# Kernel optimization log

Measured on AMD Instinct MI355X. Metric: run time of the kernel, lower is better.

Reference implementation:

```python
import jax, jax.numpy as jnp
import numpy as np

D_MODEL = 1024
NUM_HEADS = 16
D_HEAD = D_MODEL // NUM_HEADS
MAX_DISTANCE = 128
SEQ_LEN = 2048


def setup_inputs() -> dict:
    key = jax.random.key(0)
    k_x, k_qkv, k_out, k_bias = jax.random.split(key, 4)
    scale = 1.0 / np.sqrt(D_MODEL)
    return {
        "x": jax.random.normal(k_x, (SEQ_LEN, D_MODEL), dtype=jnp.float32),
        "w_qkv": jax.random.normal(k_qkv, (D_MODEL, 3 * D_MODEL), dtype=jnp.float32) * scale,
        "w_out": jax.random.normal(k_out, (D_MODEL, D_MODEL), dtype=jnp.float32) * scale,
        "rel_bias": jax.random.normal(k_bias, (MAX_DISTANCE, NUM_HEADS), dtype=jnp.float32) * 0.02,
    }


def _position_bias(rel_bias, seq_len):
    # relative_position[q, k] = k - q; bucket = clip(|rel|, 0, max_distance-1)
    ctx = jnp.arange(seq_len)[:, None]
    mem = jnp.arange(seq_len)[None, :]
    bucket = jnp.clip(jnp.abs(mem - ctx), 0, MAX_DISTANCE - 1)  # [q, k]
    return rel_bias[bucket]  # [q, k, h]


def reference(x, w_qkv, w_out, rel_bias):
    seq_len = x.shape[0]
    qkv = x @ w_qkv  # [s, 3*d_model]
    q, k, v = jnp.split(qkv, 3, axis=-1)
    q = q.reshape(seq_len, NUM_HEADS, D_HEAD)
    k = k.reshape(seq_len, NUM_HEADS, D_HEAD)
    v = v.reshape(seq_len, NUM_HEADS, D_HEAD)
    bias = _position_bias(rel_bias, seq_len)  # [q, k, h]
    # flax dot_product_attention semantics: scale q by 1/sqrt(d_head), add bias, softmax over kv
    scores = jnp.einsum("qhd,khd->hqk", q, k) / jnp.sqrt(jnp.asarray(D_HEAD, q.dtype))
    scores = scores + jnp.transpose(bias, (2, 0, 1))  # [h, q, k]
    weights = jax.nn.softmax(scores, axis=-1)
    attn = jnp.einsum("hqk,khd->qhd", weights, v)  # [s, h, d_head]
    attn = attn.reshape(1, seq_len, D_MODEL)
    return attn @ w_out  # [1, s, d_model]
```

## Files before the change

### kernel.cpp

```cpp
#include <hip/hip_runtime.h>
#include <hip/hip_bf16.h>

#define SEQ   2048
#define DM    1024
#define NH    16
#define DH    64
#define MAXD  128

#define LOG2E 1.44269504f

typedef __attribute__((ext_vector_type(8))) short  short8;
typedef __attribute__((ext_vector_type(4))) float  float4v;

__device__ __forceinline__ short8 ld8(const void* p) {
    short8 v; __builtin_memcpy(&v, p, 16); return v;
}
__device__ __forceinline__ void st8(void* p, short8 v) {
    __builtin_memcpy(p, &v, 16);
}
__device__ __forceinline__ short bf16bits(float f) {
    __hip_bfloat16 b = __float2bfloat16(f);
    short s; __builtin_memcpy(&s, &b, 2); return s;
}
__device__ __forceinline__ short bf16fast(float f) {
    unsigned u = __builtin_bit_cast(unsigned, f);
    return (short)((u + 0x8000u) >> 16);
}
__device__ __forceinline__ float bits2f(short s) {
    unsigned u = (unsigned)(unsigned short)s << 16;
    return __builtin_bit_cast(float, u);
}
__device__ __forceinline__ short fp16bits(float f) {
    _Float16 h = (_Float16)f; short s; __builtin_memcpy(&s, &h, 2); return s;
}
__device__ __forceinline__ float f16tof(short s) {
    _Float16 h; __builtin_memcpy(&h, &s, 2); return (float)h;
}
__device__ __forceinline__ float fexp2(float x) {
    float r; asm("v_exp_f32 %0, %1" : "=v"(r) : "v"(x)); return r;
}

__device__ __forceinline__ void async16(void* lds, const void* g) {
    __builtin_amdgcn_global_load_lds(
        (const __attribute__((address_space(1))) unsigned int*)g,
        (__attribute__((address_space(3))) unsigned int*)lds, 16, 0, 0);
}

template <int CTRL>
__device__ __forceinline__ float dppmov(float x) {
    return __builtin_bit_cast(float,
        __builtin_amdgcn_update_dpp(0, __builtin_bit_cast(int, x), CTRL, 0xf, 0xf, true));
}
__device__ __forceinline__ float red16max(float x) {
    x = fmaxf(x, dppmov<0xB1>(x));
    x = fmaxf(x, dppmov<0x4E>(x));
    x = fmaxf(x, dppmov<0x141>(x));
    x = fmaxf(x, dppmov<0x140>(x));
    return x;
}
__device__ __forceinline__ float red16sum(float x) {
    x += dppmov<0xB1>(x);
    x += dppmov<0x4E>(x);
    x += dppmov<0x141>(x);
    x += dppmov<0x140>(x);
    return x;
}

__global__ __launch_bounds__(256) void prep_kernel(
    const float* __restrict__ wq, const float* __restrict__ wo,
    const float* __restrict__ x,
    __hip_bfloat16* __restrict__ wqT, __hip_bfloat16* __restrict__ woT,
    __hip_bfloat16* __restrict__ xb) {
    const int t = threadIdx.x;
    const int bx = blockIdx.x;
    if (bx >= 128) {
        const size_t id = (size_t)(bx - 128) * 32 + blockIdx.y;
        const size_t i  = id * 2048 + t * 8;
        float f[8]; __builtin_memcpy(f, x + i, 32);
        short8 v;
#pragma unroll
        for (int j = 0; j < 8; ++j) v[j] = bf16bits(f[j]);
        st8(xb + i, v);
        return;
    }
    __shared__ __hip_bfloat16 tile[32][33];
    const int tx = t % 32, ty = t / 32;
    const int r0 = blockIdx.y * 32;
    const float* src; __hip_bfloat16* dst; int ss, ds, c0;
    if (bx < 96) { src = wq; dst = wqT; ss = 3 * DM; ds = DM; c0 = bx * 32; }
    else         { src = wo; dst = woT; ss = DM;     ds = DM; c0 = (bx - 96) * 32; }
#pragma unroll
    for (int i = 0; i < 4; ++i)
        tile[ty + i * 8][tx] = __float2bfloat16(src[(size_t)(r0 + ty + i * 8) * ss + c0 + tx]);
    __syncthreads();
#pragma unroll
    for (int i = 0; i < 4; ++i)
        dst[(size_t)(c0 + ty + i * 8) * ds + r0 + tx] = tile[tx][ty + i * 8];
}

__global__ __launch_bounds__(256) void gemm_qkv(
    const __hip_bfloat16* __restrict__ A,
    const __hip_bfloat16* __restrict__ BT,
    __hip_bfloat16* __restrict__ C,
    __hip_bfloat16* __restrict__ vTg,
    int M, int N, int K) {
    __shared__ short As[2 * 128 * 32];
    __shared__ short Bs[2 * 64 * 32];
    __shared__ short Tv[64 * 132];

    const int t = threadIdx.x;
    const int w = t >> 6, lane = t & 63;
    const int l15 = lane & 15, quad = lane >> 4;
    const int row0 = blockIdx.y * 128;
    const int col0 = blockIdx.x * 64;
    const int wm = w >> 1, wn = w & 1;

    float4v acc[4][2];
#pragma unroll
    for (int i = 0; i < 4; ++i)
#pragma unroll
        for (int j = 0; j < 2; ++j) acc[i][j] = (float4v){0.f, 0.f, 0.f, 0.f};

    const int mloc0 = lane >> 2;
    const int u     = lane & 3;

    for (int k0 = 0; k0 < K; k0 += 64) {
#pragma unroll
        for (int kc = 0; kc < 2; ++kc) {
#pragma unroll
            for (int i = 0; i < 2; ++i) {
                const int c = 2 * w + i;
                async16(&As[kc * 4096 + c * 512],
                        A + (size_t)(row0 + c * 16 + mloc0) * K + k0 + kc * 32 + u * 8);
            }
            async16(&Bs[kc * 2048 + w * 512],
                    BT + (size_t)(col0 + w * 16 + mloc0) * K + k0 + kc * 32 + u * 8);
        }
        __syncthreads();

#pragma unroll
        for (int kc = 0; kc < 2; ++kc) {
            short8 af[4], bf[2];
#pragma unroll
            for (int mt = 0; mt < 4; ++mt)
                af[mt] = ld8(&As[kc * 4096 + (wm * 64 + mt * 16 + l15) * 32 + quad * 8]);
#pragma unroll
            for (int nt = 0; nt < 2; ++nt)
                bf[nt] = ld8(&Bs[kc * 2048 + (wn * 32 + nt * 16 + l15) * 32 + quad * 8]);
#pragma unroll
            for (int mt = 0; mt < 4; ++mt)
#pragma unroll
                for (int nt = 0; nt < 2; ++nt)
                    acc[mt][nt] = __builtin_amdgcn_mfma_f32_16x16x32_bf16(
                        af[mt], bf[nt], acc[mt][nt], 0, 0, 0);
        }
        __syncthreads();
    }

    if (col0 < 2 * DM) {
#pragma unroll
        for (int mt = 0; mt < 4; ++mt)
#pragma unroll
            for (int nt = 0; nt < 2; ++nt)
#pragma unroll
                for (int r = 0; r < 4; ++r) {
                    const int row = row0 + wm * 64 + mt * 16 + quad * 4 + r;
                    const int col = col0 + wn * 32 + nt * 16 + l15;
                    C[(size_t)row * N + col] = __float2bfloat16(acc[mt][nt][r]);
                }
    } else {
#pragma unroll
        for (int mt = 0; mt < 4; ++mt)
#pragma unroll
            for (int nt = 0; nt < 2; ++nt)
#pragma unroll
                for (int r = 0; r < 4; ++r)
                    Tv[(wn * 32 + nt * 16 + l15) * 132 + wm * 64 + mt * 16 + quad * 4 + r] =
                        bf16bits(acc[mt][nt][r]);
        __syncthreads();
#pragma unroll
        for (int p = 0; p < 4; ++p) {
            const int idx = p * 256 + t;
            const int dl = idx >> 4, uu = idx & 15;
            st8(&vTg[((size_t)(col0 - 2 * DM) + dl) * SEQ + row0 + uu * 8],
                ld8(&Tv[dl * 132 + uu * 8]));
        }
    }
}

__global__ __launch_bounds__(256) void gemm_out(
    const __hip_bfloat16* __restrict__ A,
    const __hip_bfloat16* __restrict__ BT,
    float* __restrict__ C,
    int M, int N, int K) {
    __shared__ short As[2 * 64 * 32];
    __shared__ short Bs[2 * 64 * 32];

    const int t = threadIdx.x;
    const int w = t >> 6, lane = t & 63;
    const int l15 = lane & 15, quad = lane >> 4;
    const int row0 = blockIdx.y * 64;
    const int col0 = blockIdx.x * 64;
    const int wm = w >> 1, wn = w & 1;

    float4v acc[2][2];
#pragma unroll
    for (int i = 0; i < 2; ++i)
#pragma unroll
        for (int j = 0; j < 2; ++j) acc[i][j] = (float4v){0.f, 0.f, 0.f, 0.f};

    const int mloc0 = lane >> 2;
    const int u     = lane & 3;

    for (int k0 = 0; k0 < K; k0 += 64) {
#pragma unroll
        for (int kc = 0; kc < 2; ++kc) {
            async16(&As[kc * 2048 + w * 512],
                    A + (size_t)(row0 + w * 16 + mloc0) * K + k0 + kc * 32 + u * 8);
            async16(&Bs[kc * 2048 + w * 512],
                    BT + (size_t)(col0 + w * 16 + mloc0) * K + k0 + kc * 32 + u * 8);
        }
        __syncthreads();

#pragma unroll
        for (int kc = 0; kc < 2; ++kc) {
            short8 af[2], bf[2];
#pragma unroll
            for (int mt = 0; mt < 2; ++mt)
                af[mt] = ld8(&As[kc * 2048 + (wm * 32 + mt * 16 + l15) * 32 + quad * 8]);
#pragma unroll
            for (int nt = 0; nt < 2; ++nt)
                bf[nt] = ld8(&Bs[kc * 2048 + (wn * 32 + nt * 16 + l15) * 32 + quad * 8]);
#pragma unroll
            for (int mt = 0; mt < 2; ++mt)
#pragma unroll
                for (int nt = 0; nt < 2; ++nt)
                    acc[mt][nt] = __builtin_amdgcn_mfma_f32_16x16x32_bf16(
                        af[mt], bf[nt], acc[mt][nt], 0, 0, 0);
        }
        __syncthreads();
    }

#pragma unroll
    for (int mt = 0; mt < 2; ++mt)
#pragma unroll
        for (int nt = 0; nt < 2; ++nt)
#pragma unroll
            for (int r = 0; r < 4; ++r) {
                const int row = row0 + wm * 32 + mt * 16 + quad * 4 + r;
                const int col = col0 + wn * 32 + nt * 16 + l15;
                C[(size_t)row * N + col] = acc[mt][nt][r];
            }
}

#define TK    128
#define NTILE (SEQ / 2 / TK)
#define KS    68
#define VS    132

__global__ __launch_bounds__(256) void attn_part(
    const __hip_bfloat16* __restrict__ qkv,
    const __hip_bfloat16* __restrict__ vT,
    const float* __restrict__ rel_bias,
    short* __restrict__ opart,
    float* __restrict__ ml) {
    __shared__ short KtPl[TK * KS];
    __shared__ short Vt[DH * VS];
    __shared__ float biasL[MAXD];

    const int t = threadIdx.x;
    const int w = t >> 6, lane = t & 63;
    const int l15 = lane & 15, quad = lane >> 4;

    const int id = blockIdx.x;
    const int qb = (id >> 3) & 31;
    const int c  = (id & 7) + 8 * (id >> 8);
    const int h  = c & 15;
    const int half = c >> 4;
    const int kbase = half * (SEQ / 2);
    const int q0 = qb * 64;
    const int qw = q0 + w * 16;

    if (t < MAXD) biasL[t] = rel_bias[t * NH + h] * LOG2E;

    short8 qf[2];
#pragma unroll
    for (int cc = 0; cc < 2; ++cc) {
        short8 raw = ld8(qkv + (size_t)(qw + l15) * (3 * DM) + h * DH + cc * 32 + quad * 8);
#pragma unroll
        for (int j = 0; j < 8; ++j) qf[cc][j] = bf16bits(bits2f(raw[j]) * (0.125f * LOG2E));
    }

    float4v o_acc[4];
#pragma unroll
    for (int nt = 0; nt < 4; ++nt) o_acc[nt] = (float4v){0.f, 0.f, 0.f, 0.f};
    float m_i[4], l_i[4];
#pragma unroll
    for (int r = 0; r < 4; ++r) { m_i[r] = -1e30f; l_i[r] = 0.f; }

    for (int kb = 0; kb < NTILE; ++kb) {
        const int k0 = kbase + kb * TK;
#pragma unroll
        for (int p = 0; p < 4; ++p) {
            const int idx = p * 256 + t;
            const int row = idx >> 3, u = idx & 7;
            st8(&KtPl[row * KS + u * 8],
                ld8(qkv + (size_t)(k0 + row) * (3 * DM) + DM + h * DH + u * 8));
        }
#pragma unroll
        for (int p = 0; p < 4; ++p) {
            const int idx = p * 256 + t;
            const int row = idx >> 4, u = idx & 15;
            st8(&Vt[row * VS + u * 8],
                ld8(vT + (size_t)(h * DH + row) * SEQ + k0 + u * 8));
        }
        __syncthreads();

        float4v s_acc[8];
#pragma unroll
        for (int kt = 0; kt < 8; ++kt) s_acc[kt] = (float4v){0.f, 0.f, 0.f, 0.f};
#pragma unroll
        for (int cc = 0; cc < 2; ++cc)
#pragma unroll
            for (int kt = 0; kt < 8; ++kt) {
                short8 kf = ld8(&KtPl[(kt * 16 + l15) * KS + (cc * 4 + quad) * 8]);
                s_acc[kt] = __builtin_amdgcn_mfma_f32_16x16x32_bf16(qf[cc], kf, s_acc[kt], 0, 0, 0);
            }

        float sv[8][4];
        const int dlo = k0 - (qw + 15);
        const int dhi = qw - (k0 + TK - 1);
        if (dlo >= MAXD - 1 || dhi >= MAXD - 1) {
            const float bu = biasL[MAXD - 1];
#pragma unroll
            for (int kt = 0; kt < 8; ++kt)
#pragma unroll
                for (int r = 0; r < 4; ++r) sv[kt][r] = s_acc[kt][r] + bu;
        } else {
#pragma unroll
            for (int kt = 0; kt < 8; ++kt)
#pragma unroll
                for (int r = 0; r < 4; ++r) {
                    const int kg = k0 + kt * 16 + l15;
                    const int qg = qw + quad * 4 + r;
                    int rel = kg - qg; if (rel < 0) rel = -rel;
                    if (rel > MAXD - 1) rel = MAXD - 1;
                    sv[kt][r] = s_acc[kt][r] + biasL[rel];
                }
        }

        float rowm[4];
#pragma unroll
        for (int r = 0; r < 4; ++r) {
            float m = sv[0][r];
#pragma unroll
            for (int kt = 1; kt < 8; ++kt) m = fmaxf(m, sv[kt][r]);
            rowm[r] = red16max(m);
        }

        float al[4], rs[4];
#pragma unroll
        for (int r = 0; r < 4; ++r) {
            const float mn = fmaxf(m_i[r], rowm[r]);
            al[r] = fexp2(m_i[r] - mn);
            m_i[r] = mn;
            rs[r] = 0.f;
        }
#pragma unroll
        for (int kt = 0; kt < 8; ++kt)
#pragma unroll
            for (int r = 0; r < 4; ++r) {
                const float p = fexp2(sv[kt][r] - m_i[r]);
                sv[kt][r] = p;
                rs[r] += p;
            }
#pragma unroll
        for (int r = 0; r < 4; ++r) {
            rs[r] = red16sum(rs[r]);
            l_i[r] = l_i[r] * al[r] + rs[r];
        }
#pragma unroll
        for (int nt = 0; nt < 4; ++nt)
#pragma unroll
            for (int r = 0; r < 4; ++r) o_acc[nt][r] *= al[r];

        __syncthreads();

#pragma unroll
        for (int kt = 0; kt < 8; ++kt)
#pragma unroll
            for (int r = 0; r < 4; ++r)
                KtPl[w * 16 * VS + (quad * 4 + r) * VS + kt * 16 + l15] = bf16fast(sv[kt][r]);

#pragma unroll
        for (int kc = 0; kc < 4; ++kc) {
            short8 pf = ld8(&KtPl[w * 16 * VS + l15 * VS + kc * 32 + quad * 8]);
#pragma unroll
            for (int nt = 0; nt < 4; ++nt) {
                short8 vf = ld8(&Vt[(nt * 16 + l15) * VS + kc * 32 + quad * 8]);
                o_acc[nt] = __builtin_amdgcn_mfma_f32_16x16x32_bf16(pf, vf, o_acc[nt], 0, 0, 0);
            }
        }
        __syncthreads();
    }

#pragma unroll
    for (int nt = 0; nt < 4; ++nt)
#pragma unroll
        for (int r = 0; r < 4; ++r) {
            const int row = qw + quad * 4 + r;
            const int col = h * DH + nt * 16 + l15;
            opart[((size_t)half * SEQ + row) * DM + col] = fp16bits(o_acc[nt][r] / l_i[r]);
        }
    if (l15 == 0) {
#pragma unroll
        for (int r = 0; r < 4; ++r) {
            const int row = qw + quad * 4 + r;
            float* mp = ml + (((size_t)half * SEQ + row) * NH + h) * 2;
            mp[0] = m_i[r];
            mp[1] = l_i[r];
        }
    }
}

__global__ __launch_bounds__(256) void combine_kernel(
    const short* __restrict__ opart,
    const float* __restrict__ ml,
    __hip_bfloat16* __restrict__ attnb) {
    const size_t e = ((size_t)blockIdx.x * 256 + threadIdx.x) * 8;
    const int row = (int)(e >> 10);
    const int c0  = (int)(e & 1023);
    const int h   = c0 >> 6;

    const float* mp1 = ml + ((size_t)row * NH + h) * 2;
    const float* mp2 = mp1 + (size_t)SEQ * NH * 2;
    const float m1 = mp1[0], l1 = mp1[1];
    const float m2 = mp2[0], l2 = mp2[1];
    const float mx = fmaxf(m1, m2);
    const float e1 = fexp2(m1 - mx) * l1;
    const float e2 = fexp2(m2 - mx) * l2;
    const float inv = 1.f / (e1 + e2);
    const float w1 = e1 * inv, w2 = e2 * inv;

    short8 a = ld8(opart + (size_t)row * DM + c0);
    short8 b = ld8(opart + (size_t)SEQ * DM + (size_t)row * DM + c0);
    short8 o;
#pragma unroll
    for (int j = 0; j < 8; ++j)
        o[j] = bf16bits(w1 * f16tof(a[j]) + w2 * f16tof(b[j]));
    st8(attnb + (size_t)row * DM + c0, o);
}

extern "C" void kernel_launch(void* const* d_in, const int* in_sizes, int n_in,
                              void* d_out, int out_size, void* d_ws, size_t ws_size,
                              hipStream_t stream) {
    const float* x        = (const float*)d_in[0];
    const float* w_qkv    = (const float*)d_in[1];
    const float* w_out    = (const float*)d_in[2];
    const float* rel_bias = (const float*)d_in[3];
    float* out = (float*)d_out;

    char* p = (char*)d_ws;
    __hip_bfloat16* xb    = (__hip_bfloat16*)p;  p += (size_t)SEQ * DM * 2;
    __hip_bfloat16* wqT   = (__hip_bfloat16*)p;  p += (size_t)3 * DM * DM * 2;
    __hip_bfloat16* woT   = (__hip_bfloat16*)p;  p += (size_t)DM * DM * 2;
    __hip_bfloat16* qkvb  = (__hip_bfloat16*)p;  p += (size_t)SEQ * 3 * DM * 2;
    __hip_bfloat16* vT    = (__hip_bfloat16*)p;  p += (size_t)DM * SEQ * 2;
    __hip_bfloat16* attnb = (__hip_bfloat16*)p;

    short* opart = (short*)d_ws;
    float* ml    = (float*)((char*)d_ws + (size_t)2 * SEQ * DM * 2);

    prep_kernel<<<dim3(160, 32), 256, 0, stream>>>(w_qkv, w_out, x, wqT, woT, xb);

    gemm_qkv<<<dim3(3 * DM / 64, SEQ / 128), 256, 0, stream>>>(
        xb, wqT, qkvb, vT, SEQ, 3 * DM, DM);

    attn_part<<<1024, 256, 0, stream>>>(qkvb, vT, rel_bias, opart, ml);
    combine_kernel<<<1024, 256, 0, stream>>>(opart, ml, attnb);

    gemm_out<<<dim3(DM / 64, SEQ / 64), 256, 0, stream>>>(
        attnb, woT, out, SEQ, DM, DM);
}
```

Baseline: 167.6 us.

## Process 32 query rows per wave with transposed MFMA in split-KV attention

```diff
diff --git a/kernel.cpp b/kernel.cpp
--- a/kernel.cpp
+++ b/kernel.cpp
@@ -22,16 +22,20 @@
     __hip_bfloat16 b = __float2bfloat16(f);
     short s; __builtin_memcpy(&s, &b, 2); return s;
 }
-__device__ __forceinline__ short bf16fast(float f) {
-    unsigned u = __builtin_bit_cast(unsigned, f);
-    return (short)((u + 0x8000u) >> 16);
-}
 __device__ __forceinline__ float bits2f(short s) {
     unsigned u = (unsigned)(unsigned short)s << 16;
     return __builtin_bit_cast(float, u);
 }
-__device__ __forceinline__ short fp16bits(float f) {
-    _Float16 h = (_Float16)f; short s; __builtin_memcpy(&s, &h, 2); return s;
+__device__ __forceinline__ unsigned packbf2(float a, float b) {
+    unsigned ua = (__builtin_bit_cast(unsigned, a) + 0x8000u) >> 16;
+    unsigned ub = (__builtin_bit_cast(unsigned, b) + 0x8000u) & 0xffff0000u;
+    return ua | ub;
+}
+__device__ __forceinline__ unsigned packh2(float a, float b) {
+    _Float16 ha = (_Float16)a, hb = (_Float16)b;
+    unsigned short ua, ub;
+    __builtin_memcpy(&ua, &ha, 2); __builtin_memcpy(&ub, &hb, 2);
+    return (unsigned)ua | ((unsigned)ub << 16);
 }
 __device__ __forceinline__ float f16tof(short s) {
     _Float16 h; __builtin_memcpy(&h, &s, 2); return (float)h;
@@ -44,26 +48,6 @@
     __builtin_amdgcn_global_load_lds(
         (const __attribute__((address_space(1))) unsigned int*)g,
         (__attribute__((address_space(3))) unsigned int*)lds, 16, 0, 0);
-}
-
-template <int CTRL>
-__device__ __forceinline__ float dppmov(float x) {
-    return __builtin_bit_cast(float,
-        __builtin_amdgcn_update_dpp(0, __builtin_bit_cast(int, x), CTRL, 0xf, 0xf, true));
-}
-__device__ __forceinline__ float red16max(float x) {
-    x = fmaxf(x, dppmov<0xB1>(x));
-    x = fmaxf(x, dppmov<0x4E>(x));
-    x = fmaxf(x, dppmov<0x141>(x));
-    x = fmaxf(x, dppmov<0x140>(x));
-    return x;
-}
-__device__ __forceinline__ float red16sum(float x) {
-    x += dppmov<0xB1>(x);
-    x += dppmov<0x4E>(x);
-    x += dppmov<0x141>(x);
-    x += dppmov<0x140>(x);
-    return x;
 }
 
 __global__ __launch_bounds__(256) void prep_kernel(
@@ -257,14 +241,15 @@
 #define NTILE (SEQ / 2 / TK)
 #define KS    68
 #define VS    132
-
-__global__ __launch_bounds__(256) void attn_part(
+#define PS    140
+
+__global__ __launch_bounds__(256, 2) void attn_part(
     const __hip_bfloat16* __restrict__ qkv,
     const __hip_bfloat16* __restrict__ vT,
     const float* __restrict__ rel_bias,
     short* __restrict__ opart,
     float* __restrict__ ml) {
-    __shared__ short KtPl[TK * KS];
+    __shared__ short KtP[4 * 32 * PS];
     __shared__ short Vt[DH * VS];
     __shared__ float biasL[MAXD];
 
@@ -273,30 +258,33 @@
     const int l15 = lane & 15, quad = lane >> 4;
 
     const int id = blockIdx.x;
-    const int qb = (id >> 3) & 31;
-    const int c  = (id & 7) + 8 * (id >> 8);
+    const int qb = (id >> 3) & 15;
+    const int c  = (id & 7) + 8 * (id >> 7);
     const int h  = c & 15;
     const int half = c >> 4;
     const int kbase = half * (SEQ / 2);
-    const int q0 = qb * 64;
-    const int qw = q0 + w * 16;
+    const int qw = qb * 128 + w * 32;
 
     if (t < MAXD) biasL[t] = rel_bias[t * NH + h] * LOG2E;
 
-    short8 qf[2];
-#pragma unroll
-    for (int cc = 0; cc < 2; ++cc) {
-        short8 raw = ld8(qkv + (size_t)(qw + l15) * (3 * DM) + h * DH + cc * 32 + quad * 8);
-#pragma unroll
-        for (int j = 0; j < 8; ++j) qf[cc][j] = bf16bits(bits2f(raw[j]) * (0.125f * LOG2E));
-    }
-
-    float4v o_acc[4];
-#pragma unroll
-    for (int nt = 0; nt < 4; ++nt) o_acc[nt] = (float4v){0.f, 0.f, 0.f, 0.f};
-    float m_i[4], l_i[4];
-#pragma unroll
-    for (int r = 0; r < 4; ++r) { m_i[r] = -1e30f; l_i[r] = 0.f; }
+    short8 qf[2][2];
+#pragma unroll
+    for (int qg = 0; qg < 2; ++qg)
+#pragma unroll
+        for (int cc = 0; cc < 2; ++cc) {
+            short8 raw = ld8(qkv + (size_t)(qw + qg * 16 + l15) * (3 * DM) + h * DH + cc * 32 + quad * 8);
+#pragma unroll
+            for (int j = 0; j < 8; ++j) qf[qg][cc][j] = bf16bits(bits2f(raw[j]) * (0.125f * LOG2E));
+        }
+
+    float4v o_acc[4][2];
+#pragma unroll
+    for (int nt = 0; nt < 4; ++nt)
+#pragma unroll
+        for (int qg = 0; qg < 2; ++qg) o_acc[nt][qg] = (float4v){0.f, 0.f, 0.f, 0.f};
+    float m_i[2] = {-1e30f, -1e30f}, l_i[2] = {0.f, 0.f};
+
+    short* Pw = &KtP[w * 32 * PS];
 
     for (int kb = 0; kb < NTILE; ++kb) {
         const int k0 = kbase + kb * TK;
@@ -304,7 +292,7 @@
         for (int p = 0; p < 4; ++p) {
             const int idx = p * 256 + t;
             const int row = idx >> 3, u = idx & 7;
-            st8(&KtPl[row * KS + u * 8],
+            st8(&KtP[row * KS + u * 8],
                 ld8(qkv + (size_t)(k0 + row) * (3 * DM) + DM + h * DH + u * 8));
         }
 #pragma unroll
@@ -316,109 +304,130 @@
         }
         __syncthreads();
 
-        float4v s_acc[8];
-#pragma unroll
-        for (int kt = 0; kt < 8; ++kt) s_acc[kt] = (float4v){0.f, 0.f, 0.f, 0.f};
+        float4v s_acc[2][8];
+#pragma unroll
+        for (int qg = 0; qg < 2; ++qg)
+#pragma unroll
+            for (int kt = 0; kt < 8; ++kt) s_acc[qg][kt] = (float4v){0.f, 0.f, 0.f, 0.f};
 #pragma unroll
         for (int cc = 0; cc < 2; ++cc)
 #pragma unroll
             for (int kt = 0; kt < 8; ++kt) {
-                short8 kf = ld8(&KtPl[(kt * 16 + l15) * KS + (cc * 4 + quad) * 8]);
-                s_acc[kt] = __builtin_amdgcn_mfma_f32_16x16x32_bf16(qf[cc], kf, s_acc[kt], 0, 0, 0);
-            }
-
-        float sv[8][4];
-        const int dlo = k0 - (qw + 15);
+                short8 kf = ld8(&KtP[(kt * 16 + l15) * KS + (cc * 4 + quad) * 8]);
+                s_acc[0][kt] = __builtin_amdgcn_mfma_f32_16x16x32_bf16(kf, qf[0][cc], s_acc[0][kt], 0, 0, 0);
+                s_acc[1][kt] = __builtin_amdgcn_mfma_f32_16x16x32_bf16(kf, qf[1][cc], s_acc[1][kt], 0, 0, 0);
+            }
+
+        const int dlo = k0 - (qw + 31);
         const int dhi = qw - (k0 + TK - 1);
         if (dlo >= MAXD - 1 || dhi >= MAXD - 1) {
             const float bu = biasL[MAXD - 1];
 #pragma unroll
+            for (int qg = 0; qg < 2; ++qg)
+#pragma unroll
+                for (int kt = 0; kt < 8; ++kt)
+#pragma unroll
+                    for (int r = 0; r < 4; ++r) s_acc[qg][kt][r] += bu;
+        } else {
+#pragma unroll
+            for (int qg = 0; qg < 2; ++qg) {
+                const int qrow = qw + qg * 16 + l15;
+#pragma unroll
+                for (int kt = 0; kt < 8; ++kt)
+#pragma unroll
+                    for (int r = 0; r < 4; ++r) {
+                        const int kg = k0 + kt * 16 + quad * 4 + r;
+                        int rel = kg - qrow; if (rel < 0) rel = -rel;
+                        if (rel > MAXD - 1) rel = MAXD - 1;
+                        s_acc[qg][kt][r] += biasL[rel];
+                    }
+            }
+        }
+
+        float al[2];
+#pragma unroll
+        for (int qg = 0; qg < 2; ++qg) {
+            float mk[8];
+#pragma unroll
             for (int kt = 0; kt < 8; ++kt)
-#pragma unroll
-                for (int r = 0; r < 4; ++r) sv[kt][r] = s_acc[kt][r] + bu;
-        } else {
-#pragma unroll
-            for (int kt = 0; kt < 8; ++kt)
-#pragma unroll
-                for (int r = 0; r < 4; ++r) {
-                    const int kg = k0 + kt * 16 + l15;
-                    const int qg = qw + quad * 4 + r;
-                    int rel = kg - qg; if (rel < 0) rel = -rel;
-                    if (rel > MAXD - 1) rel = MAXD - 1;
-                    sv[kt][r] = s_acc[kt][r] + biasL[rel];
-                }
-        }
-
-        float rowm[4];
-#pragma unroll
-        for (int r = 0; r < 4; ++r) {
-            float m = sv[0][r];
-#pragma unroll
-            for (int kt = 1; kt < 8; ++kt) m = fmaxf(m, sv[kt][r]);
-            rowm[r] = red16max(m);
-        }
-
-        float al[4], rs[4];
-#pragma unroll
-        for (int r = 0; r < 4; ++r) {
-            const float mn = fmaxf(m_i[r], rowm[r]);
-            al[r] = fexp2(m_i[r] - mn);
-            m_i[r] = mn;
-            rs[r] = 0.f;
-        }
-#pragma unroll
-        for (int kt = 0; kt < 8; ++kt)
-#pragma unroll
-            for (int r = 0; r < 4; ++r) {
-                const float p = fexp2(sv[kt][r] - m_i[r]);
-                sv[kt][r] = p;
-                rs[r] += p;
-            }
-#pragma unroll
-        for (int r = 0; r < 4; ++r) {
-            rs[r] = red16sum(rs[r]);
-            l_i[r] = l_i[r] * al[r] + rs[r];
+                mk[kt] = fmaxf(fmaxf(s_acc[qg][kt][0], s_acc[qg][kt][1]),
+                               fmaxf(s_acc[qg][kt][2], s_acc[qg][kt][3]));
+            float m = fmaxf(fmaxf(fmaxf(mk[0], mk[1]), fmaxf(mk[2], mk[3])),
+                            fmaxf(fmaxf(mk[4], mk[5]), fmaxf(mk[6], mk[7])));
+            m = fmaxf(m, __shfl_xor(m, 16, 64));
+            m = fmaxf(m, __shfl_xor(m, 32, 64));
+            const float mn = fmaxf(m_i[qg], m);
+            al[qg] = fexp2(m_i[qg] - mn);
+            m_i[qg] = mn;
+            float sk[8];
+#pragma unroll
+            for (int kt = 0; kt < 8; ++kt) {
+                float p0 = fexp2(s_acc[qg][kt][0] - mn);
+                float p1 = fexp2(s_acc[qg][kt][1] - mn);
+                float p2 = fexp2(s_acc[qg][kt][2] - mn);
+                float p3 = fexp2(s_acc[qg][kt][3] - mn);
+                s_acc[qg][kt][0] = p0; s_acc[qg][kt][1] = p1;
+                s_acc[qg][kt][2] = p2; s_acc[qg][kt][3] = p3;
+                sk[kt] = (p0 + p1) + (p2 + p3);
+            }
+            float rs = ((sk[0] + sk[1]) + (sk[2] + sk[3])) +
+                       ((sk[4] + sk[5]) + (sk[6] + sk[7]));
+            rs += __shfl_xor(rs, 16, 64);
+            rs += __shfl_xor(rs, 32, 64);
+            l_i[qg] = l_i[qg] * al[qg] + rs;
         }
 #pragma unroll
         for (int nt = 0; nt < 4; ++nt)
 #pragma unroll
-            for (int r = 0; r < 4; ++r) o_acc[nt][r] *= al[r];
-
-        __syncthreads();
-
-#pragma unroll
-        for (int kt = 0; kt < 8; ++kt)
-#pragma unroll
-            for (int r = 0; r < 4; ++r)
-                KtPl[w * 16 * VS + (quad * 4 + r) * VS + kt * 16 + l15] = bf16fast(sv[kt][r]);
+            for (int qg = 0; qg < 2; ++qg)
+#pragma unroll
+                for (int r = 0; r < 4; ++r) o_acc[nt][qg][r] *= al[qg];
+
+        __syncthreads();
+
+#pragma unroll
+        for (int qg = 0; qg < 2; ++qg)
+#pragma unroll
+            for (int kt = 0; kt < 8; ++kt) {
+                unsigned d0 = packbf2(s_acc[qg][kt][0], s_acc[qg][kt][1]);
+                unsigned d1 = packbf2(s_acc[qg][kt][2], s_acc[qg][kt][3]);
+                unsigned long long v = (unsigned long long)d0 | ((unsigned long long)d1 << 32);
+                __builtin_memcpy(&Pw[(qg * 16 + l15) * PS + kt * 16 + quad * 4], &v, 8);
+            }
 
 #pragma unroll
         for (int kc = 0; kc < 4; ++kc) {
-            short8 pf = ld8(&KtPl[w * 16 * VS + l15 * VS + kc * 32 + quad * 8]);
+            short8 pf0 = ld8(&Pw[l15 * PS + kc * 32 + quad * 8]);
+            short8 pf1 = ld8(&Pw[(16 + l15) * PS + kc * 32 + quad * 8]);
 #pragma unroll
             for (int nt = 0; nt < 4; ++nt) {
                 short8 vf = ld8(&Vt[(nt * 16 + l15) * VS + kc * 32 + quad * 8]);
-                o_acc[nt] = __builtin_amdgcn_mfma_f32_16x16x32_bf16(pf, vf, o_acc[nt], 0, 0, 0);
-            }
-        }
-        __syncthreads();
-    }
-
-#pragma unroll
-    for (int nt = 0; nt < 4; ++nt)
-#pragma unroll
-        for (int r = 0; r < 4; ++r) {
-            const int row = qw + quad * 4 + r;
-            const int col = h * DH + nt * 16 + l15;
-            opart[((size_t)half * SEQ + row) * DM + col] = fp16bits(o_acc[nt][r] / l_i[r]);
-        }
-    if (l15 == 0) {
-#pragma unroll
-        for (int r = 0; r < 4; ++r) {
-            const int row = qw + quad * 4 + r;
-            float* mp = ml + (((size_t)half * SEQ + row) * NH + h) * 2;
-            mp[0] = m_i[r];
-            mp[1] = l_i[r];
+                o_acc[nt][0] = __builtin_amdgcn_mfma_f32_16x16x32_bf16(vf, pf0, o_acc[nt][0], 0, 0, 0);
+                o_acc[nt][1] = __builtin_amdgcn_mfma_f32_16x16x32_bf16(vf, pf1, o_acc[nt][1], 0, 0, 0);
+            }
+        }
+        __syncthreads();
+    }
+
+#pragma unroll
+    for (int qg = 0; qg < 2; ++qg) {
+        const float inv = 1.f / l_i[qg];
+        const int qrow = qw + qg * 16 + l15;
+#pragma unroll
+        for (int nt = 0; nt < 4; ++nt) {
+            unsigned d0 = packh2(o_acc[nt][qg][0] * inv, o_acc[nt][qg][1] * inv);
+            unsigned d1 = packh2(o_acc[nt][qg][2] * inv, o_acc[nt][qg][3] * inv);
+            unsigned long long v = (unsigned long long)d0 | ((unsigned long long)d1 << 32);
+            __builtin_memcpy(opart + ((size_t)half * SEQ + qrow) * DM + h * DH + nt * 16 + quad * 4, &v, 8);
+        }
+    }
+    if (quad == 0) {
+#pragma unroll
+        for (int qg = 0; qg < 2; ++qg) {
+            const int qrow = qw + qg * 16 + l15;
+            float* mp = ml + (((size_t)half * SEQ + qrow) * NH + h) * 2;
+            mp[0] = m_i[qg];
+            mp[1] = l_i[qg];
         }
     }
 }
@@ -476,7 +485,7 @@
     gemm_qkv<<<dim3(3 * DM / 64, SEQ / 128), 256, 0, stream>>>(
         xb, wqT, qkvb, vT, SEQ, 3 * DM, DM);
 
-    attn_part<<<1024, 256, 0, stream>>>(qkvb, vT, rel_bias, opart, ml);
+    attn_part<<<512, 256, 0, stream>>>(qkvb, vT, rel_bias, opart, ml);
     combine_kernel<<<1024, 256, 0, stream>>>(opart, ml, attnb);
 
     gemm_out<<<dim3(DM / 64, SEQ / 64), 256, 0, stream>>>(
```

Measured after the change: 153.1 us. 8.7% less time.
